# Kernel tuning notes

Hardware: AMD Instinct MI355X
Metric: run time of the kernel (lower is better)

The kernel has to match this reference:

```python
import jax, jax.numpy as jnp
import numpy as np

B, C, H = 64, 64, 32

def _pm_cross_pairs(ks):
    # Replicates PM_cross(2, ks): pairs (i, i+j) ordered by gap j=1..ks-1, then i.
    a, b = [], []
    for j in range(1, ks):
        for i in range(ks - j):
            a.append(i)
            b.append(i + j)
    return np.array(a, dtype=np.int32), np.array(b, dtype=np.int32)

def setup_inputs() -> dict:
    key = jax.random.key(0)
    k1, k2 = jax.random.split(key)
    ia, ib = _pm_cross_pairs(H)           # 496 pairs for H=32
    hk = ia.shape[0] + 2 * H              # 560
    x = jax.random.normal(k1, (B, C, H, H), dtype=jnp.float32)
    weight = 0.1 * jax.random.normal(k2, (C, H, hk, H), dtype=jnp.float32)
    return {"x": x, "weight": weight, "idx_a": jnp.asarray(ia), "idx_b": jnp.asarray(ib)}

def reference(x, weight, idx_a, idx_b):
    # cross-term products along last axis: [B,C,H,P]
    cross = x[..., idx_a] * x[..., idx_b]
    feat = jnp.concatenate([x, x * x, cross], axis=-1)  # [B,C,H,Hk]
    # per-(channel,row) grouped matmul
    return jnp.einsum('bcij,cijo->bcio', feat, weight)
```

## Files before the change

kernel.cpp:

```cpp
#include <hip/hip_runtime.h>

#define NB 64
#define NC 64
#define NH 32
#define HK 560
#define XSTR 57

typedef __bf16 bf16x8 __attribute__((ext_vector_type(8)));
typedef float f32x4 __attribute__((ext_vector_type(4)));

__global__ __launch_bounds__(256, 4) void hconv_kernel(
    const float* __restrict__ x, const float* __restrict__ w,
    const int* __restrict__ idx_a, const int* __restrict__ idx_b,
    float* __restrict__ out)
{
    __shared__ __align__(16) float smem[4 * 64 * 33];
    float* s_x = smem;
    float* s_stage = &smem[NB * XSTR];

    const int t = threadIdx.x;
    const int g = blockIdx.x;
    const int c = g >> 5, i = g & 31;

    const int wv = t >> 6, lane = t & 63;
    const int lr = lane & 15, lq = lane >> 4;
    const float* wbase = w + (size_t)(c * NH + i) * HK * NH;

    const int xrow = t >> 2, seg = t & 3;
    const float* xr = x + (((size_t)xrow * NC + c) * NH + i) * NH + seg * 8;
    float4 v0 = *(const float4*)(xr);
    float4 v1 = *(const float4*)(xr + 4);

    unsigned d6[6];
    #pragma unroll
    for (int k = 0; k < 6; ++k) {
        const int mm = (k >> 1) * 8 + (k & 1) * 4 + lq;
        const int q = mm * 4 + wv;
        unsigned pa, pb, ko;
        if (mm >= 21)   { pa = 0u; pb = 0u; ko = 0u; }
        else if (q < 4) { pa = 8u + 8u * q; pb = 48u; ko = 8u * q; }
        else if (q < 8) { unsigned u = q - 4; pa = pb = 8u + 8u * u; ko = 32u + 8u * u; }
        else {
            unsigned qq = q - 8, j, a;
            if (qq < 28)      { j = 1 + qq / 4;         a = qq % 4; }
            else if (qq < 52) { j = 8 + (qq - 28) / 3;  a = (qq - 28) % 3; }
            else if (qq < 68) { j = 16 + (qq - 52) / 2; a = (qq - 52) % 2; }
            else              { j = 24 + (qq - 68);     a = 0; }
            ko = 64u + (j - 1) * 32u - (j * (j - 1)) / 2u + 8u * a;
            pa = 8u + 8u * a; pb = pa + j;
            if (ko > 552u) { unsigned sh = ko - 552u; ko = 552u; pa -= sh; pb -= sh; }
        }
        d6[k] = pa | (pb << 6) | (ko << 12);
    }

    f32x4 gA[4], gB[4], gC[4];

#define GLOAD(G, K) { \
    _Pragma("unroll") \
    for (int o_ = 0; o_ < 4; ++o_) { \
        unsigned dd_ = (unsigned)__builtin_amdgcn_readlane((int)d6[K], 16 * o_); \
        const float* wp_ = wbase + (size_t)(dd_ >> 12) * NH + 4 * lane; \
        G[o_] = *(const f32x4*)wp_; } }

    GLOAD(gA, 0);
    GLOAD(gB, 1);
    GLOAD(gC, 2);

    {
        float* dst = &s_x[xrow * XSTR + 8 + seg * 8];
        dst[0] = v0.x; dst[1] = v0.y; dst[2] = v0.z; dst[3] = v0.w;
        dst[4] = v1.x; dst[5] = v1.y; dst[6] = v1.z; dst[7] = v1.w;
        if (seg == 0) {
            float* r0 = &s_x[xrow * XSTR];
            #pragma unroll
            for (int m = 0; m < 8; ++m) {
                r0[m] = 0.0f;
                r0[40 + m] = 0.0f;
                r0[48 + m] = 1.0f;
            }
        }
    }

    f32x4 acc[4][2];
    #pragma unroll
    for (int r = 0; r < 4; ++r) {
        acc[r][0] = (f32x4){0.f, 0.f, 0.f, 0.f};
        acc[r][1] = (f32x4){0.f, 0.f, 0.f, 0.f};
    }

#define SWRITE(G) { \
    float* tb_ = s_stage + wv * 1056 + (lane >> 3) * 33 + (lane & 7) * 4; \
    _Pragma("unroll") \
    for (int o_ = 0; o_ < 4; ++o_) \
        _Pragma("unroll") \
        for (int w_ = 0; w_ < 4; ++w_) \
            tb_[o_ * 264 + w_] = G[o_][w_]; }

#define STEP(K, DOLD, GLD, DOWR, GWR) { \
    bf16x8 b0_, b1_; \
    { const float* rb_ = s_stage + wv * 1056 + lq * 264 + lr; \
      _Pragma("unroll") \
      for (int j_ = 0; j_ < 8; ++j_) { \
          b0_[j_] = (__bf16)rb_[j_ * 33]; \
          b1_[j_] = (__bf16)rb_[j_ * 33 + 16]; } } \
    if (DOLD) GLOAD(GLD, (K) + 3); \
    if (DOWR) SWRITE(GWR); \
    const unsigned d_ = d6[K]; \
    _Pragma("unroll") \
    for (int rt_ = 0; rt_ < 4; ++rt_) { \
        const float* xr_ = &s_x[(rt_ * 16 + lr) * XSTR]; \
        const float* qa_ = xr_ + (d_ & 63u); \
        const float* qb_ = xr_ + ((d_ >> 6) & 63u); \
        bf16x8 a_; \
        _Pragma("unroll") \
        for (int j_ = 0; j_ < 8; ++j_) a_[j_] = (__bf16)(qa_[j_] * qb_[j_]); \
        acc[rt_][0] = __builtin_amdgcn_mfma_f32_16x16x32_bf16(a_, b0_, acc[rt_][0], 0, 0, 0); \
        acc[rt_][1] = __builtin_amdgcn_mfma_f32_16x16x32_bf16(a_, b1_, acc[rt_][1], 0, 0, 0); } }

    __syncthreads();

    SWRITE(gA);
    STEP(0, 1, gA, 1, gB);
    STEP(1, 1, gB, 1, gC);
    STEP(2, 1, gC, 1, gA);
    STEP(3, 0, gA, 1, gB);
    STEP(4, 0, gA, 1, gC);
    STEP(5, 0, gA, 0, gA);

#undef STEP
#undef SWRITE
#undef GLOAD

    __syncthreads();

    #pragma unroll
    for (int rt = 0; rt < 4; ++rt)
        #pragma unroll
        for (int nh = 0; nh < 2; ++nh)
            #pragma unroll
            for (int r = 0; r < 4; ++r)
                smem[(wv * NB + rt * 16 + lq * 4 + r) * 33 + nh * 16 + lr] =
                    acc[rt][nh][r];

    __syncthreads();

    {
        const int b = t >> 2, m0 = (t & 3) * 8;
        float s0[8];
        #pragma unroll
        for (int m = 0; m < 8; ++m) s0[m] = smem[b * 33 + m0 + m];
        #pragma unroll
        for (int wv2 = 1; wv2 < 4; ++wv2)
            #pragma unroll
            for (int m = 0; m < 8; ++m)
                s0[m] += smem[(wv2 * NB + b) * 33 + m0 + m];
        float* op = out + (((size_t)b * NC + c) * NH + i) * NH + m0;
        float4 o0 = {s0[0], s0[1], s0[2], s0[3]};
        float4 o1 = {s0[4], s0[5], s0[6], s0[7]};
        *(float4*)op = o0;
        *(float4*)(op + 4) = o1;
    }
}

extern "C" void kernel_launch(void* const* d_in, const int* in_sizes, int n_in,
                              void* d_out, int out_size, void* d_ws, size_t ws_size,
                              hipStream_t stream) {
    const float* x = (const float*)d_in[0];
    const float* w = (const float*)d_in[1];
    const int* idx_a = (const int*)d_in[2];
    const int* idx_b = (const int*)d_in[3];
    float* out = (float*)d_out;
    hconv_kernel<<<dim3(NC * NH), dim3(256), 0, stream>>>(x, w, idx_a, idx_b, out);
}
```

Baseline: 232.5 us.

## Reassign cross-term chunks to lanes, stage weights as bf16, cache x rows in registers

Rebuilds the per-lane assignment of 8-wide feature chunks so that in the first four steps each lane's left operand is a fixed x segment. That segment is hoisted into registers, so only one shared-memory operand is read per product. Weight staging in LDS now stores bf16 instead of fp32, which halves staging traffic and removes conversions on read. Empty chunks are marked with a sentinel so their global loads are skipped, and only two register buffers are used instead of three, which cuts register pressure. The hand-written assignment table is intricate and mistakes would silently give wrong results.

```diff
diff --git a/kernel.cpp b/kernel.cpp
--- a/kernel.cpp
+++ b/kernel.cpp
@@ -16,7 +16,7 @@
 {
     __shared__ __align__(16) float smem[4 * 64 * 33];
     float* s_x = smem;
-    float* s_stage = &smem[NB * XSTR];
+    unsigned short* s_wtu = (unsigned short*)&smem[NB * XSTR];
 
     const int t = threadIdx.x;
     const int g = blockIdx.x;
@@ -25,46 +25,85 @@
     const int wv = t >> 6, lane = t & 63;
     const int lr = lane & 15, lq = lane >> 4;
     const float* wbase = w + (size_t)(c * NH + i) * HK * NH;
-
     const int xrow = t >> 2, seg = t & 3;
     const float* xr = x + (((size_t)xrow * NC + c) * NH + i) * NH + seg * 8;
+
     float4 v0 = *(const float4*)(xr);
     float4 v1 = *(const float4*)(xr + 4);
 
+#define BLK(J) ((unsigned)(64 + ((J) - 1) * 32 - ((J) * ((J) - 1)) / 2))
     unsigned d6[6];
     #pragma unroll
-    for (int k = 0; k < 6; ++k) {
-        const int mm = (k >> 1) * 8 + (k & 1) * 4 + lq;
-        const int q = mm * 4 + wv;
+    for (int st = 0; st < 6; ++st) {
         unsigned pa, pb, ko;
-        if (mm >= 21)   { pa = 0u; pb = 0u; ko = 0u; }
-        else if (q < 4) { pa = 8u + 8u * q; pb = 48u; ko = 8u * q; }
-        else if (q < 8) { unsigned u = q - 4; pa = pb = 8u + 8u * u; ko = 32u + 8u * u; }
-        else {
-            unsigned qq = q - 8, j, a;
-            if (qq < 28)      { j = 1 + qq / 4;         a = qq % 4; }
-            else if (qq < 52) { j = 8 + (qq - 28) / 3;  a = (qq - 28) % 3; }
-            else if (qq < 68) { j = 16 + (qq - 52) / 2; a = (qq - 52) % 2; }
-            else              { j = 24 + (qq - 68);     a = 0; }
-            ko = 64u + (j - 1) * 32u - (j * (j - 1)) / 2u + 8u * a;
-            pa = 8u + 8u * a; pb = pa + j;
-            if (ko > 552u) { unsigned sh = ko - 552u; ko = 552u; pa -= sh; pb -= sh; }
+        if (st < 4) {
+            pa = 8u + 8u * (unsigned)lq;
+            if (lq <= 1) {
+                const int j = wv * 4 + st + 1;
+                pb = pa + (unsigned)j; ko = BLK(j) + 8u * (unsigned)lq;
+            } else if (lq == 2) {
+                if (wv == 3 && st == 3) { pb = 24u; ko = 48u; }
+                else { const int j = wv * 4 + st + 1;
+                       pb = 24u + (unsigned)j; ko = BLK(j) + 16u; }
+            } else {
+                if (wv == 0) { const int j = st + 1; pb = 32u + (unsigned)j; ko = BLK(j) + 24u; }
+                else if (wv == 1) {
+                    if (st < 3) { const int j = st + 5; pb = 32u + (unsigned)j; ko = BLK(j) + 24u; }
+                    else        { pb = 32u; ko = 56u; }
+                } else if (wv == 2) {
+                    if (st == 0) { pb = 48u; ko = 24u; }
+                    else         { pb = 48u; ko = 1023u; }
+                } else               { pb = 48u; ko = 1023u; }
+            }
+        } else if (st == 4) {
+            if (wv == 0)      { const int j = 17 + lq; pa = 8u;  pb = 8u + (unsigned)j;  ko = BLK(j); }
+            else if (wv == 1) { const int j = 22 + lq; pa = 8u;  pb = 8u + (unsigned)j;  ko = BLK(j); }
+            else if (wv == 2) {
+                if (lq == 0)      { pa = 8u; pb = 36u; ko = 550u; }
+                else if (lq == 1) { pa = 6u; pb = 35u; ko = 552u; }
+                else if (lq == 2) { pa = 3u; pb = 33u; ko = 552u; }
+                else              { pa = 1u; pb = 32u; ko = 552u; }
+            } else            { const int j = 17 + lq; pa = 16u; pb = 16u + (unsigned)j; ko = BLK(j) + 8u; }
+        } else {
+            if (wv == 0) {
+                if (lq == 0) { pa = 8u; pb = 29u; ko = BLK(21); }
+                else         { pa = 0u; pb = 0u;  ko = 1023u; }
+            } else if (wv == 1) {
+                if (lq == 0)      { pa = 8u; pb = 34u; ko = BLK(26); }
+                else if (lq == 1) { pa = 8u; pb = 35u; ko = BLK(27); }
+                else              { pa = 0u; pb = 0u;  ko = 1023u; }
+            } else if (wv == 2) {
+                if (lq == 0)      { pa = 8u;  pb = 8u;  ko = 32u; }
+                else if (lq == 1) { pa = 8u;  pb = 48u; ko = 0u;  }
+                else if (lq == 2) { pa = 16u; pb = 16u; ko = 40u; }
+                else              { pa = 16u; pb = 48u; ko = 8u;  }
+            } else {
+                if (lq == 0)      { pa = 16u; pb = 37u; ko = BLK(21) + 8u; }
+                else if (lq == 1) { pa = 16u; pb = 38u; ko = BLK(22) + 8u; }
+                else if (lq == 2) { pa = 16u; pb = 39u; ko = BLK(23) + 8u; }
+                else              { pa = 24u; pb = 48u; ko = 16u; }
+            }
         }
-        d6[k] = pa | (pb << 6) | (ko << 12);
-    }
-
-    f32x4 gA[4], gB[4], gC[4];
+        d6[st] = pa | (pb << 6) | (ko << 12);
+    }
+#undef BLK
+
+    f32x4 gA[4], gB[4];
 
 #define GLOAD(G, K) { \
     _Pragma("unroll") \
     for (int o_ = 0; o_ < 4; ++o_) { \
         unsigned dd_ = (unsigned)__builtin_amdgcn_readlane((int)d6[K], 16 * o_); \
-        const float* wp_ = wbase + (size_t)(dd_ >> 12) * NH + 4 * lane; \
-        G[o_] = *(const f32x4*)wp_; } }
+        unsigned ko_ = (dd_ >> 12) & 1023u; \
+        if (ko_ != 1023u) { \
+            const float* wp_ = wbase + (size_t)ko_ * NH + 4 * lane; \
+            G[o_] = *(const f32x4*)wp_; \
+        } else { \
+            G[o_] = (f32x4){0.f, 0.f, 0.f, 0.f}; \
+        } } }
 
     GLOAD(gA, 0);
     GLOAD(gB, 1);
-    GLOAD(gC, 2);
 
     {
         float* dst = &s_x[xrow * XSTR + 8 + seg * 8];
@@ -89,43 +128,58 @@
     }
 
 #define SWRITE(G) { \
-    float* tb_ = s_stage + wv * 1056 + (lane >> 3) * 33 + (lane & 7) * 4; \
+    unsigned short* tb_ = s_wtu + wv * 1088 + (lane >> 3) * 34 + (lane & 7) * 4; \
     _Pragma("unroll") \
     for (int o_ = 0; o_ < 4; ++o_) \
         _Pragma("unroll") \
         for (int w_ = 0; w_ < 4; ++w_) \
-            tb_[o_ * 264 + w_] = G[o_][w_]; }
-
-#define STEP(K, DOLD, GLD, DOWR, GWR) { \
+            tb_[o_ * 272 + w_] = \
+                __builtin_bit_cast(unsigned short, (__bf16)G[o_][w_]); \
+    asm volatile("" ::: "memory"); }
+
+    __syncthreads();
+
+    float qx[4][8];
+    #pragma unroll
+    for (int rt = 0; rt < 4; ++rt)
+        #pragma unroll
+        for (int m = 0; m < 8; ++m)
+            qx[rt][m] = s_x[(rt * 16 + lr) * XSTR + 8 + 8 * lq + m];
+
+#define STEP(ST, GEN, DOLD, GLD, DOWR, GWR) { \
     bf16x8 b0_, b1_; \
-    { const float* rb_ = s_stage + wv * 1056 + lq * 264 + lr; \
+    { const unsigned short* rb_ = s_wtu + (wv * 4 + lq) * 272 + lr; \
       _Pragma("unroll") \
       for (int j_ = 0; j_ < 8; ++j_) { \
-          b0_[j_] = (__bf16)rb_[j_ * 33]; \
-          b1_[j_] = (__bf16)rb_[j_ * 33 + 16]; } } \
-    if (DOLD) GLOAD(GLD, (K) + 3); \
+          b0_[j_] = __builtin_bit_cast(__bf16, rb_[j_ * 34]); \
+          b1_[j_] = __builtin_bit_cast(__bf16, rb_[j_ * 34 + 16]); } } \
+    if (DOLD) GLOAD(GLD, (ST) + 2); \
     if (DOWR) SWRITE(GWR); \
-    const unsigned d_ = d6[K]; \
+    const unsigned d_ = d6[ST]; \
+    const int paf_ = (int)(d_ & 63u), pbf_ = (int)((d_ >> 6) & 63u); \
     _Pragma("unroll") \
     for (int rt_ = 0; rt_ < 4; ++rt_) { \
         const float* xr_ = &s_x[(rt_ * 16 + lr) * XSTR]; \
-        const float* qa_ = xr_ + (d_ & 63u); \
-        const float* qb_ = xr_ + ((d_ >> 6) & 63u); \
+        const float* qb_ = xr_ + pbf_; \
         bf16x8 a_; \
-        _Pragma("unroll") \
-        for (int j_ = 0; j_ < 8; ++j_) a_[j_] = (__bf16)(qa_[j_] * qb_[j_]); \
+        if (GEN) { \
+            const float* qa_ = xr_ + paf_; \
+            _Pragma("unroll") \
+            for (int j_ = 0; j_ < 8; ++j_) a_[j_] = (__bf16)(qa_[j_] * qb_[j_]); \
+        } else { \
+            _Pragma("unroll") \
+            for (int j_ = 0; j_ < 8; ++j_) a_[j_] = (__bf16)(qx[rt_][j_] * qb_[j_]); \
+        } \
         acc[rt_][0] = __builtin_amdgcn_mfma_f32_16x16x32_bf16(a_, b0_, acc[rt_][0], 0, 0, 0); \
         acc[rt_][1] = __builtin_amdgcn_mfma_f32_16x16x32_bf16(a_, b1_, acc[rt_][1], 0, 0, 0); } }
 
-    __syncthreads();
-
     SWRITE(gA);
-    STEP(0, 1, gA, 1, gB);
-    STEP(1, 1, gB, 1, gC);
-    STEP(2, 1, gC, 1, gA);
-    STEP(3, 0, gA, 1, gB);
-    STEP(4, 0, gA, 1, gC);
-    STEP(5, 0, gA, 0, gA);
+    STEP(0, 0, 1, gA, 1, gB);
+    STEP(1, 0, 1, gB, 1, gA);
+    STEP(2, 0, 1, gA, 1, gB);
+    STEP(3, 0, 1, gB, 1, gA);
+    STEP(4, 1, 0, gA, 1, gB);
+    STEP(5, 1, 0, gA, 0, gA);
 
 #undef STEP
 #undef SWRITE
```

Measured after the change: 236.8 us. Within noise of the previous version (+1.8%).
